# Kernel tuning notes

Hardware: AMD Instinct MI355X
Metric: run time of the kernel (lower is better)

The kernel has to match this reference:

```python
import jax, jax.numpy as jnp
import numpy as np

TAU = 1.0   # ltc_params['tau_constant']
DT = 0.1    # LTCCell default dt
UNFOLDS = 6 # ltc_params['ode_unfolds']
B, S, D, H, O = 512, 512, 128, 128, 1


def setup_inputs() -> dict:
    key = jax.random.key(0)
    ks = jax.random.split(key, 7)
    sc = lambda n: 1.0 / np.sqrt(n)
    return {
        "x":    jax.random.normal(ks[0], (B, S, D), dtype=jnp.float32),
        "W_in": jax.random.normal(ks[1], (H, D), dtype=jnp.float32) * sc(D),
        "b_in": jax.random.normal(ks[2], (H,), dtype=jnp.float32) * sc(D),
        "W_r":  jax.random.normal(ks[3], (H, H), dtype=jnp.float32) * sc(H),
        "b_r":  jax.random.normal(ks[4], (H,), dtype=jnp.float32) * sc(H),
        "W_fc": jax.random.normal(ks[5], (O, H), dtype=jnp.float32) * sc(H),
        "b_fc": jax.random.normal(ks[6], (O,), dtype=jnp.float32) * sc(H),
    }


def reference(x, W_in, b_in, W_r, b_r, W_fc, b_fc):
    # input_map(x[:, t]) is invariant across the inner unfold loop -> precompute once.
    xin_all = jnp.einsum('bsd,hd->bsh', x, W_in) + b_in  # [B,S,H]

    def step(h, xin):  # h: [B,H], xin: [B,H]
        for _ in range(UNFOLDS):  # small fixed count, unrolled
            v = jnp.tanh(xin + h @ W_r.T + b_r)
            h = h + DT * (-h / TAU + v)
        return h, None

    h0 = jnp.zeros((x.shape[0], W_r.shape[0]), dtype=x.dtype)
    h, _ = jax.lax.scan(step, h0, jnp.swapaxes(xin_all, 0, 1))  # scan over seq
    return (h @ W_fc.T + b_fc).squeeze(-1)  # [B]
```

## Files before the change

kernel.cpp:

```cpp
#include <hip/hip_runtime.h>


typedef _Float16 v2h __attribute__((ext_vector_type(2)));

#define S_LEN 512
#define HDIM 128
#define NUNF 6
#define DTC 0.1f

__device__ __forceinline__ float fast_tanh(float y) {
    float u = __expf(2.0f * y);
    return 1.0f - __fdividef(2.0f, u + 1.0f);
}

__global__ __launch_bounds__(256, 2)
void ltc_kernel(const float* __restrict__ x,
                const float* __restrict__ W_in,
                const float* __restrict__ b_in,
                const float* __restrict__ W_r,
                const float* __restrict__ b_r,
                const float* __restrict__ W_fc,
                const float* __restrict__ b_fc,
                float* __restrict__ out)
{
    const int b     = blockIdx.x;
    const int tid   = threadIdx.x;
    const int o     = tid >> 1;
    const int kh    = tid & 1;
    const int kbase = kh * 64;

    __shared__ __align__(16) _Float16 hbuf[2][HDIM];
    __shared__ __align__(16) _Float16 xbuf[2][HDIM];
    __shared__ float red[4];

    v2h wr[32], wi[32];
    {
        const float4* wrp = reinterpret_cast<const float4*>(W_r  + o * HDIM + kbase);
        const float4* wip = reinterpret_cast<const float4*>(W_in + o * HDIM + kbase);
#pragma unroll
        for (int j = 0; j < 16; ++j) {
            float4 f = wrp[j];
            wr[2*j]   = v2h{(_Float16)f.x, (_Float16)f.y};
            wr[2*j+1] = v2h{(_Float16)f.z, (_Float16)f.w};
            float4 g = wip[j];
            wi[2*j]   = v2h{(_Float16)g.x, (_Float16)g.y};
            wi[2*j+1] = v2h{(_Float16)g.z, (_Float16)g.w};
        }
    }
    const float binv = b_in[o];
    const float brv  = b_r[o];

    const float* x_row = x + (size_t)b * S_LEN * HDIM;

    float h_o = 0.0f;

    if (tid < HDIM) {
        xbuf[0][tid] = (_Float16)x_row[tid];
        hbuf[0][tid] = (_Float16)0.0f;
    }
    __syncthreads();

    for (int s = 0; s < S_LEN; ++s) {
        float xnext = 0.0f;
        if (tid < HDIM && s + 1 < S_LEN)
            xnext = x_row[(size_t)(s + 1) * HDIM + tid];

        float xin_o;
        {
            const float4* hp = reinterpret_cast<const float4*>(&xbuf[s & 1][kbase]);
            float4 hv[8];
#pragma unroll
            for (int j = 0; j < 8; ++j) hv[j] = hp[j];
            const v2h* hh = reinterpret_cast<const v2h*>(hv);
            float a0 = 0.f, a1 = 0.f, a2 = 0.f, a3 = 0.f;
#pragma unroll
            for (int j = 0; j < 32; j += 4) {
                a0 = __builtin_amdgcn_fdot2(wi[j],   hh[j],   a0, false);
                a1 = __builtin_amdgcn_fdot2(wi[j+1], hh[j+1], a1, false);
                a2 = __builtin_amdgcn_fdot2(wi[j+2], hh[j+2], a2, false);
                a3 = __builtin_amdgcn_fdot2(wi[j+3], hh[j+3], a3, false);
            }
            float sum = (a0 + a1) + (a2 + a3);
            sum += __shfl_xor(sum, 1);
            xin_o = sum + binv;
        }

#pragma unroll
        for (int u = 0; u < NUNF; ++u) {
            const float4* hp = reinterpret_cast<const float4*>(&hbuf[u & 1][kbase]);
            float4 hv[8];
#pragma unroll
            for (int j = 0; j < 8; ++j) hv[j] = hp[j];
            const v2h* hh = reinterpret_cast<const v2h*>(hv);
            float a0 = 0.f, a1 = 0.f, a2 = 0.f, a3 = 0.f;
#pragma unroll
            for (int j = 0; j < 32; j += 4) {
                a0 = __builtin_amdgcn_fdot2(wr[j],   hh[j],   a0, false);
                a1 = __builtin_amdgcn_fdot2(wr[j+1], hh[j+1], a1, false);
                a2 = __builtin_amdgcn_fdot2(wr[j+2], hh[j+2], a2, false);
                a3 = __builtin_amdgcn_fdot2(wr[j+3], hh[j+3], a3, false);
            }
            float sum = (a0 + a1) + (a2 + a3);
            sum += __shfl_xor(sum, 1);
            float yv = xin_o + brv + sum;
            float v  = fast_tanh(yv);
            h_o = h_o + DTC * (v - h_o);
            if ((tid & 1) == 0)
                hbuf[(u + 1) & 1][o] = (_Float16)h_o;
            if (u == NUNF - 1 && tid < HDIM && s + 1 < S_LEN)
                xbuf[(s + 1) & 1][tid] = (_Float16)xnext;
            __syncthreads();
        }
    }

    float partial = 0.0f;
    if ((tid & 1) == 0) partial = h_o * W_fc[o];
#pragma unroll
    for (int d = 1; d < 64; d <<= 1) partial += __shfl_xor(partial, d);
    if ((tid & 63) == 0) red[tid >> 6] = partial;
    __syncthreads();
    if (tid == 0) out[b] = red[0] + red[1] + red[2] + red[3] + b_fc[0];
}

extern "C" void kernel_launch(void* const* d_in, const int* in_sizes, int n_in,
                              void* d_out, int out_size, void* d_ws, size_t ws_size,
                              hipStream_t stream) {
    const float* x    = (const float*)d_in[0];
    const float* W_in = (const float*)d_in[1];
    const float* b_in = (const float*)d_in[2];
    const float* W_r  = (const float*)d_in[3];
    const float* b_r  = (const float*)d_in[4];
    const float* W_fc = (const float*)d_in[5];
    const float* b_fc = (const float*)d_in[6];
    float* outp = (float*)d_out;
    (void)in_sizes; (void)n_in; (void)out_size; (void)d_ws; (void)ws_size;
    ltc_kernel<<<dim3(512), dim3(256), 0, stream>>>(x, W_in, b_in, W_r, b_r, W_fc, b_fc, outp);
}
```

Before: 1.537 ms.

## Halve block size so each thread computes two output rows

Blocks shrink from 256 to 128 threads. Each thread now holds weight slices for two output rows (o and o+64) and computes two half dot-products per step, then keeps the one matching its k-half. Barriers per block now span two wavefronts instead of four, and every thread writes h with no idle lanes. The cost is double the register weight storage (128 v2h per thread), which raises register pressure and may limit occupancy, plus twice the dot-product work per thread.

```diff
diff --git a/kernel.cpp b/kernel.cpp
--- a/kernel.cpp
+++ b/kernel.cpp
@@ -13,7 +13,7 @@
     return 1.0f - __fdividef(2.0f, u + 1.0f);
 }
 
-__global__ __launch_bounds__(256, 2)
+__global__ __launch_bounds__(128, 2)
 void ltc_kernel(const float* __restrict__ x,
                 const float* __restrict__ W_in,
                 const float* __restrict__ b_in,
@@ -25,64 +25,68 @@
 {
     const int b     = blockIdx.x;
     const int tid   = threadIdx.x;
-    const int o     = tid >> 1;
+    const int og    = tid >> 1;
     const int kh    = tid & 1;
     const int kbase = kh * 64;
+    const int o0    = og;
+    const int o1    = og + 64;
+    const int od    = kh ? o1 : o0;
 
     __shared__ __align__(16) _Float16 hbuf[2][HDIM];
     __shared__ __align__(16) _Float16 xbuf[2][HDIM];
-    __shared__ float red[4];
+    __shared__ float red[2];
 
-    v2h wr[32], wi[32];
+    v2h wr0[32], wr1[32], wi0[32], wi1[32];
     {
-        const float4* wrp = reinterpret_cast<const float4*>(W_r  + o * HDIM + kbase);
-        const float4* wip = reinterpret_cast<const float4*>(W_in + o * HDIM + kbase);
+        const float4* wr0p = reinterpret_cast<const float4*>(W_r  + o0 * HDIM + kbase);
+        const float4* wr1p = reinterpret_cast<const float4*>(W_r  + o1 * HDIM + kbase);
+        const float4* wi0p = reinterpret_cast<const float4*>(W_in + o0 * HDIM + kbase);
+        const float4* wi1p = reinterpret_cast<const float4*>(W_in + o1 * HDIM + kbase);
 #pragma unroll
         for (int j = 0; j < 16; ++j) {
-            float4 f = wrp[j];
-            wr[2*j]   = v2h{(_Float16)f.x, (_Float16)f.y};
-            wr[2*j+1] = v2h{(_Float16)f.z, (_Float16)f.w};
-            float4 g = wip[j];
-            wi[2*j]   = v2h{(_Float16)g.x, (_Float16)g.y};
-            wi[2*j+1] = v2h{(_Float16)g.z, (_Float16)g.w};
+            float4 f;
+            f = wr0p[j]; wr0[2*j] = v2h{(_Float16)f.x,(_Float16)f.y}; wr0[2*j+1] = v2h{(_Float16)f.z,(_Float16)f.w};
+            f = wr1p[j]; wr1[2*j] = v2h{(_Float16)f.x,(_Float16)f.y}; wr1[2*j+1] = v2h{(_Float16)f.z,(_Float16)f.w};
+            f = wi0p[j]; wi0[2*j] = v2h{(_Float16)f.x,(_Float16)f.y}; wi0[2*j+1] = v2h{(_Float16)f.z,(_Float16)f.w};
+            f = wi1p[j]; wi1[2*j] = v2h{(_Float16)f.x,(_Float16)f.y}; wi1[2*j+1] = v2h{(_Float16)f.z,(_Float16)f.w};
         }
     }
-    const float binv = b_in[o];
-    const float brv  = b_r[o];
+    const float binv = b_in[od];
+    const float brv  = b_r[od];
 
     const float* x_row = x + (size_t)b * S_LEN * HDIM;
 
-    float h_o = 0.0f;
+    float h_d = 0.0f;
 
-    if (tid < HDIM) {
-        xbuf[0][tid] = (_Float16)x_row[tid];
-        hbuf[0][tid] = (_Float16)0.0f;
-    }
+    xbuf[0][tid] = (_Float16)x_row[tid];
+    hbuf[0][tid] = (_Float16)0.0f;
     __syncthreads();
 
     for (int s = 0; s < S_LEN; ++s) {
         float xnext = 0.0f;
-        if (tid < HDIM && s + 1 < S_LEN)
+        if (s + 1 < S_LEN)
             xnext = x_row[(size_t)(s + 1) * HDIM + tid];
 
-        float xin_o;
+        float xin_d;
         {
             const float4* hp = reinterpret_cast<const float4*>(&xbuf[s & 1][kbase]);
             float4 hv[8];
 #pragma unroll
             for (int j = 0; j < 8; ++j) hv[j] = hp[j];
             const v2h* hh = reinterpret_cast<const v2h*>(hv);
-            float a0 = 0.f, a1 = 0.f, a2 = 0.f, a3 = 0.f;
+            float a0 = 0.f, a1 = 0.f, b0 = 0.f, b1 = 0.f;
 #pragma unroll
-            for (int j = 0; j < 32; j += 4) {
-                a0 = __builtin_amdgcn_fdot2(wi[j],   hh[j],   a0, false);
-                a1 = __builtin_amdgcn_fdot2(wi[j+1], hh[j+1], a1, false);
-                a2 = __builtin_amdgcn_fdot2(wi[j+2], hh[j+2], a2, false);
-                a3 = __builtin_amdgcn_fdot2(wi[j+3], hh[j+3], a3, false);
+            for (int j = 0; j < 32; j += 2) {
+                a0 = __builtin_amdgcn_fdot2(wi0[j],   hh[j],   a0, false);
+                a1 = __builtin_amdgcn_fdot2(wi0[j+1], hh[j+1], a1, false);
+                b0 = __builtin_amdgcn_fdot2(wi1[j],   hh[j],   b0, false);
+                b1 = __builtin_amdgcn_fdot2(wi1[j+1], hh[j+1], b1, false);
             }
-            float sum = (a0 + a1) + (a2 + a3);
-            sum += __shfl_xor(sum, 1);
-            xin_o = sum + binv;
+            float p0 = a0 + a1;
+            float p1 = b0 + b1;
+            float f0 = p0 + __shfl_xor(p0, 1);
+            float f1 = p1 + __shfl_xor(p1, 1);
+            xin_d = (kh ? f1 : f0) + binv;
         }
 
 #pragma unroll
@@ -92,34 +96,34 @@
 #pragma unroll
             for (int j = 0; j < 8; ++j) hv[j] = hp[j];
             const v2h* hh = reinterpret_cast<const v2h*>(hv);
-            float a0 = 0.f, a1 = 0.f, a2 = 0.f, a3 = 0.f;
+            float a0 = 0.f, a1 = 0.f, b0 = 0.f, b1 = 0.f;
 #pragma unroll
-            for (int j = 0; j < 32; j += 4) {
-                a0 = __builtin_amdgcn_fdot2(wr[j],   hh[j],   a0, false);
-                a1 = __builtin_amdgcn_fdot2(wr[j+1], hh[j+1], a1, false);
-                a2 = __builtin_amdgcn_fdot2(wr[j+2], hh[j+2], a2, false);
-                a3 = __builtin_amdgcn_fdot2(wr[j+3], hh[j+3], a3, false);
+            for (int j = 0; j < 32; j += 2) {
+                a0 = __builtin_amdgcn_fdot2(wr0[j],   hh[j],   a0, false);
+                a1 = __builtin_amdgcn_fdot2(wr0[j+1], hh[j+1], a1, false);
+                b0 = __builtin_amdgcn_fdot2(wr1[j],   hh[j],   b0, false);
+                b1 = __builtin_amdgcn_fdot2(wr1[j+1], hh[j+1], b1, false);
             }
-            float sum = (a0 + a1) + (a2 + a3);
-            sum += __shfl_xor(sum, 1);
-            float yv = xin_o + brv + sum;
+            float p0 = a0 + a1;
+            float p1 = b0 + b1;
+            float f0 = p0 + __shfl_xor(p0, 1);
+            float f1 = p1 + __shfl_xor(p1, 1);
+            float yv = xin_d + brv + (kh ? f1 : f0);
             float v  = fast_tanh(yv);
-            h_o = h_o + DTC * (v - h_o);
-            if ((tid & 1) == 0)
-                hbuf[(u + 1) & 1][o] = (_Float16)h_o;
-            if (u == NUNF - 1 && tid < HDIM && s + 1 < S_LEN)
+            h_d = h_d + DTC * (v - h_d);
+            hbuf[(u + 1) & 1][od] = (_Float16)h_d;
+            if (u == NUNF - 1 && s + 1 < S_LEN)
                 xbuf[(s + 1) & 1][tid] = (_Float16)xnext;
             __syncthreads();
         }
     }
 
-    float partial = 0.0f;
-    if ((tid & 1) == 0) partial = h_o * W_fc[o];
+    float partial = h_d * W_fc[od];
 #pragma unroll
     for (int d = 1; d < 64; d <<= 1) partial += __shfl_xor(partial, d);
     if ((tid & 63) == 0) red[tid >> 6] = partial;
     __syncthreads();
-    if (tid == 0) out[b] = red[0] + red[1] + red[2] + red[3] + b_fc[0];
+    if (tid == 0) out[b] = red[0] + red[1] + b_fc[0];
 }
 
 extern "C" void kernel_launch(void* const* d_in, const int* in_sizes, int n_in,
@@ -134,5 +138,5 @@
     const float* b_fc = (const float*)d_in[6];
     float* outp = (float*)d_out;
     (void)in_sizes; (void)n_in; (void)out_size; (void)d_ws; (void)ws_size;
-    ltc_kernel<<<dim3(512), dim3(256), 0, stream>>>(x, W_in, b_in, W_r, b_r, W_fc, b_fc, outp);
+    ltc_kernel<<<dim3(512), dim3(128), 0, stream>>>(x, W_in, b_in, W_r, b_r, W_fc, b_fc, outp);
 }
```

Result: slower. 1.804 ms (+17.4%).

## Run each batch row on a single wavefront to drop block barriers

Applied to the files above, without the earlier changes.

Each batch row is now handled by one 64-lane wavefront instead of a 256-thread block. Each lane computes two full-length output rows with the fp16 weights held in registers. This removes the per-unfold __syncthreads, the cross-lane shuffle and the double-buffered shared memory, which were serialising the recurrence. In exchange each wave does four times the dot-product work per step, fewer waves are resident per CU, and the roughly 256 VGPRs of weights raise register pressure and the risk of spills.

```diff
diff --git a/kernel.cpp b/kernel.cpp
--- a/kernel.cpp
+++ b/kernel.cpp
@@ -13,7 +13,7 @@
     return 1.0f - __fdividef(2.0f, u + 1.0f);
 }
 
-__global__ __launch_bounds__(256, 2)
+__global__ __launch_bounds__(64, 1)
 void ltc_kernel(const float* __restrict__ x,
                 const float* __restrict__ W_in,
                 const float* __restrict__ b_in,
@@ -23,103 +23,113 @@
                 const float* __restrict__ b_fc,
                 float* __restrict__ out)
 {
-    const int b     = blockIdx.x;
-    const int tid   = threadIdx.x;
-    const int o     = tid >> 1;
-    const int kh    = tid & 1;
-    const int kbase = kh * 64;
+    const int b  = blockIdx.x;
+    const int ln = threadIdx.x;
+    const int o0 = ln;
+    const int o1 = ln + 64;
 
-    __shared__ __align__(16) _Float16 hbuf[2][HDIM];
-    __shared__ __align__(16) _Float16 xbuf[2][HDIM];
-    __shared__ float red[4];
+    __shared__ __align__(16) _Float16 hbuf[HDIM];
+    __shared__ __align__(16) _Float16 xbuf[HDIM];
 
-    v2h wr[32], wi[32];
+    v2h wr0[64], wr1[64], wi0[64], wi1[64];
     {
-        const float4* wrp = reinterpret_cast<const float4*>(W_r  + o * HDIM + kbase);
-        const float4* wip = reinterpret_cast<const float4*>(W_in + o * HDIM + kbase);
+        const float2* r0 = reinterpret_cast<const float2*>(W_r  + o0 * HDIM);
+        const float2* r1 = reinterpret_cast<const float2*>(W_r  + o1 * HDIM);
+        const float2* i0 = reinterpret_cast<const float2*>(W_in + o0 * HDIM);
+        const float2* i1 = reinterpret_cast<const float2*>(W_in + o1 * HDIM);
 #pragma unroll
-        for (int j = 0; j < 16; ++j) {
-            float4 f = wrp[j];
-            wr[2*j]   = v2h{(_Float16)f.x, (_Float16)f.y};
-            wr[2*j+1] = v2h{(_Float16)f.z, (_Float16)f.w};
-            float4 g = wip[j];
-            wi[2*j]   = v2h{(_Float16)g.x, (_Float16)g.y};
-            wi[2*j+1] = v2h{(_Float16)g.z, (_Float16)g.w};
+        for (int p = 0; p < 64; ++p) {
+            float2 f;
+            f = r0[p]; wr0[p] = v2h{(_Float16)f.x, (_Float16)f.y};
+            f = r1[p]; wr1[p] = v2h{(_Float16)f.x, (_Float16)f.y};
+            f = i0[p]; wi0[p] = v2h{(_Float16)f.x, (_Float16)f.y};
+            f = i1[p]; wi1[p] = v2h{(_Float16)f.x, (_Float16)f.y};
         }
     }
-    const float binv = b_in[o];
-    const float brv  = b_r[o];
+    const float bi0 = b_in[o0], bi1 = b_in[o1];
+    const float br0 = b_r[o0],  br1 = b_r[o1];
 
     const float* x_row = x + (size_t)b * S_LEN * HDIM;
 
-    float h_o = 0.0f;
+    float h0 = 0.0f, h1 = 0.0f;
 
-    if (tid < HDIM) {
-        xbuf[0][tid] = (_Float16)x_row[tid];
-        hbuf[0][tid] = (_Float16)0.0f;
-    }
-    __syncthreads();
+    xbuf[o0] = (_Float16)x_row[o0];
+    xbuf[o1] = (_Float16)x_row[o1];
+    hbuf[o0] = (_Float16)0.0f;
+    hbuf[o1] = (_Float16)0.0f;
 
     for (int s = 0; s < S_LEN; ++s) {
-        float xnext = 0.0f;
-        if (tid < HDIM && s + 1 < S_LEN)
-            xnext = x_row[(size_t)(s + 1) * HDIM + tid];
+        float xn0 = 0.0f, xn1 = 0.0f;
+        if (s + 1 < S_LEN) {
+            const float* xr = x_row + (size_t)(s + 1) * HDIM;
+            xn0 = xr[o0];
+            xn1 = xr[o1];
+        }
 
-        float xin_o;
+        float xin0, xin1;
         {
-            const float4* hp = reinterpret_cast<const float4*>(&xbuf[s & 1][kbase]);
-            float4 hv[8];
+            const float4* xp = reinterpret_cast<const float4*>(xbuf);
+            float4 hv[16];
 #pragma unroll
-            for (int j = 0; j < 8; ++j) hv[j] = hp[j];
+            for (int j = 0; j < 16; ++j) hv[j] = xp[j];
             const v2h* hh = reinterpret_cast<const v2h*>(hv);
             float a0 = 0.f, a1 = 0.f, a2 = 0.f, a3 = 0.f;
+            float c0 = 0.f, c1 = 0.f, c2 = 0.f, c3 = 0.f;
 #pragma unroll
-            for (int j = 0; j < 32; j += 4) {
-                a0 = __builtin_amdgcn_fdot2(wi[j],   hh[j],   a0, false);
-                a1 = __builtin_amdgcn_fdot2(wi[j+1], hh[j+1], a1, false);
-                a2 = __builtin_amdgcn_fdot2(wi[j+2], hh[j+2], a2, false);
-                a3 = __builtin_amdgcn_fdot2(wi[j+3], hh[j+3], a3, false);
+            for (int p = 0; p < 64; p += 4) {
+                a0 = __builtin_amdgcn_fdot2(wi0[p],   hh[p],   a0, false);
+                a1 = __builtin_amdgcn_fdot2(wi0[p+1], hh[p+1], a1, false);
+                a2 = __builtin_amdgcn_fdot2(wi0[p+2], hh[p+2], a2, false);
+                a3 = __builtin_amdgcn_fdot2(wi0[p+3], hh[p+3], a3, false);
+                c0 = __builtin_amdgcn_fdot2(wi1[p],   hh[p],   c0, false);
+                c1 = __builtin_amdgcn_fdot2(wi1[p+1], hh[p+1], c1, false);
+                c2 = __builtin_amdgcn_fdot2(wi1[p+2], hh[p+2], c2, false);
+                c3 = __builtin_amdgcn_fdot2(wi1[p+3], hh[p+3], c3, false);
             }
-            float sum = (a0 + a1) + (a2 + a3);
-            sum += __shfl_xor(sum, 1);
-            xin_o = sum + binv;
+            xin0 = (a0 + a1) + (a2 + a3) + bi0;
+            xin1 = (c0 + c1) + (c2 + c3) + bi1;
         }
 
 #pragma unroll
         for (int u = 0; u < NUNF; ++u) {
-            const float4* hp = reinterpret_cast<const float4*>(&hbuf[u & 1][kbase]);
-            float4 hv[8];
+            const float4* hp = reinterpret_cast<const float4*>(hbuf);
+            float4 hv[16];
 #pragma unroll
-            for (int j = 0; j < 8; ++j) hv[j] = hp[j];
+            for (int j = 0; j < 16; ++j) hv[j] = hp[j];
             const v2h* hh = reinterpret_cast<const v2h*>(hv);
             float a0 = 0.f, a1 = 0.f, a2 = 0.f, a3 = 0.f;
+            float c0 = 0.f, c1 = 0.f, c2 = 0.f, c3 = 0.f;
 #pragma unroll
-            for (int j = 0; j < 32; j += 4) {
-                a0 = __builtin_amdgcn_fdot2(wr[j],   hh[j],   a0, false);
-                a1 = __builtin_amdgcn_fdot2(wr[j+1], hh[j+1], a1, false);
-                a2 = __builtin_amdgcn_fdot2(wr[j+2], hh[j+2], a2, false);
-                a3 = __builtin_amdgcn_fdot2(wr[j+3], hh[j+3], a3, false);
+            for (int p = 0; p < 64; p += 4) {
+                a0 = __builtin_amdgcn_fdot2(wr0[p],   hh[p],   a0, false);
+                a1 = __builtin_amdgcn_fdot2(wr0[p+1], hh[p+1], a1, false);
+                a2 = __builtin_amdgcn_fdot2(wr0[p+2], hh[p+2], a2, false);
+                a3 = __builtin_amdgcn_fdot2(wr0[p+3], hh[p+3], a3, false);
+                c0 = __builtin_amdgcn_fdot2(wr1[p],   hh[p],   c0, false);
+                c1 = __builtin_amdgcn_fdot2(wr1[p+1], hh[p+1], c1, false);
+                c2 = __builtin_amdgcn_fdot2(wr1[p+2], hh[p+2], c2, false);
+                c3 = __builtin_amdgcn_fdot2(wr1[p+3], hh[p+3], c3, false);
             }
-            float sum = (a0 + a1) + (a2 + a3);
-            sum += __shfl_xor(sum, 1);
-            float yv = xin_o + brv + sum;
-            float v  = fast_tanh(yv);
-            h_o = h_o + DTC * (v - h_o);
-            if ((tid & 1) == 0)
-                hbuf[(u + 1) & 1][o] = (_Float16)h_o;
-            if (u == NUNF - 1 && tid < HDIM && s + 1 < S_LEN)
-                xbuf[(s + 1) & 1][tid] = (_Float16)xnext;
-            __syncthreads();
+            float s0 = (a0 + a1) + (a2 + a3);
+            float s1 = (c0 + c1) + (c2 + c3);
+            float v0 = fast_tanh(xin0 + br0 + s0);
+            float v1 = fast_tanh(xin1 + br1 + s1);
+            h0 = h0 + DTC * (v0 - h0);
+            h1 = h1 + DTC * (v1 - h1);
+            hbuf[o0] = (_Float16)h0;
+            hbuf[o1] = (_Float16)h1;
+        }
+
+        if (s + 1 < S_LEN) {
+            xbuf[o0] = (_Float16)xn0;
+            xbuf[o1] = (_Float16)xn1;
         }
     }
 
-    float partial = 0.0f;
-    if ((tid & 1) == 0) partial = h_o * W_fc[o];
+    float partial = h0 * W_fc[o0] + h1 * W_fc[o1];
 #pragma unroll
     for (int d = 1; d < 64; d <<= 1) partial += __shfl_xor(partial, d);
-    if ((tid & 63) == 0) red[tid >> 6] = partial;
-    __syncthreads();
-    if (tid == 0) out[b] = red[0] + red[1] + red[2] + red[3] + b_fc[0];
+    if (ln == 0) out[b] = partial + b_fc[0];
 }
 
 extern "C" void kernel_launch(void* const* d_in, const int* in_sizes, int n_in,
@@ -134,5 +144,5 @@
     const float* b_fc = (const float*)d_in[6];
     float* outp = (float*)d_out;
     (void)in_sizes; (void)n_in; (void)out_size; (void)d_ws; (void)ws_size;
-    ltc_kernel<<<dim3(512), dim3(256), 0, stream>>>(x, W_in, b_in, W_r, b_r, W_fc, b_fc, outp);
+    ltc_kernel<<<dim3(512), dim3(64), 0, stream>>>(x, W_in, b_in, W_r, b_r, W_fc, b_fc, outp);
 }
```

Result: slower. 3.204 ms (+108.4%).

## Split input projection into separate kernel and run recurrence in a single wavefront

Applied to the files above, without the earlier changes.

Moves the W_in projection out of the sequential loop into a parallel precompute kernel that writes packed fp16 pairs to workspace. The recurrence kernel then uses one 64-lane wavefront per batch row, each lane owning two hidden units, so there is no __syncthreads and no cross-lane shuffle per unfold. Instead it relies on wavefront-synchronous LDS writes and reads of the hidden state. This trades one barrier per unfold for more serial work per lane and lower occupancy (512 single-wave blocks), and assumes a workspace of 64 MB. Without that workspace it falls back to the old kernel.

```diff
diff --git a/kernel.cpp b/kernel.cpp
--- a/kernel.cpp
+++ b/kernel.cpp
@@ -5,8 +5,13 @@
 
 #define S_LEN 512
 #define HDIM 128
+#define BATCH 512
 #define NUNF 6
 #define DTC 0.1f
+
+__device__ __forceinline__ v2h pk2h(float a, float b) {
+    return __builtin_bit_cast(v2h, __builtin_amdgcn_cvt_pkrtz(a, b));
+}
 
 __device__ __forceinline__ float fast_tanh(float y) {
     float u = __expf(2.0f * y);
@@ -14,15 +19,156 @@
 }
 
 __global__ __launch_bounds__(256, 2)
-void ltc_kernel(const float* __restrict__ x,
+void xin_kernel(const float* __restrict__ x,
                 const float* __restrict__ W_in,
                 const float* __restrict__ b_in,
+                unsigned int* __restrict__ xin)
+{
+    __shared__ __align__(16) _Float16 xt[128 * HDIM];
+    const int tid  = threadIdx.x;
+    const int w    = tid >> 6;
+    const int lane = tid & 63;
+    const int bs0  = blockIdx.x * 128;
+
+    const float4* xg = reinterpret_cast<const float4*>(x + (size_t)bs0 * HDIM);
+#pragma unroll
+    for (int i = 0; i < 16; ++i) {
+        int idx = i * 1024 + tid * 4;
+        float4 v = xg[idx >> 2];
+        v2h* d = reinterpret_cast<v2h*>(xt + idx);
+        d[0] = pk2h(v.x, v.y);
+        d[1] = pk2h(v.z, v.w);
+    }
+
+    v2h wi0[64], wi1[64];
+    {
+        const float4* r0 = reinterpret_cast<const float4*>(W_in + (size_t)lane * HDIM);
+        const float4* r1 = reinterpret_cast<const float4*>(W_in + (size_t)(lane + 64) * HDIM);
+#pragma unroll
+        for (int j = 0; j < 32; ++j) {
+            float4 f = r0[j];
+            wi0[2*j]   = pk2h(f.x, f.y);
+            wi0[2*j+1] = pk2h(f.z, f.w);
+            float4 g = r1[j];
+            wi1[2*j]   = pk2h(g.x, g.y);
+            wi1[2*j+1] = pk2h(g.z, g.w);
+        }
+    }
+    const float bi0 = b_in[lane], bi1 = b_in[lane + 64];
+    __syncthreads();
+
+    for (int rr = 0; rr < 32; ++rr) {
+        const int r = w * 32 + rr;
+        const float4* hp = reinterpret_cast<const float4*>(xt + r * HDIM);
+        float a0 = 0.f, a1 = 0.f, c0 = 0.f, c1 = 0.f;
+#pragma unroll
+        for (int j = 0; j < 16; ++j) {
+            float4 q = hp[j];
+            const v2h* hh = reinterpret_cast<const v2h*>(&q);
+            a0 = __builtin_amdgcn_fdot2(wi0[4*j+0], hh[0], a0, false);
+            a1 = __builtin_amdgcn_fdot2(wi0[4*j+1], hh[1], a1, false);
+            a0 = __builtin_amdgcn_fdot2(wi0[4*j+2], hh[2], a0, false);
+            a1 = __builtin_amdgcn_fdot2(wi0[4*j+3], hh[3], a1, false);
+            c0 = __builtin_amdgcn_fdot2(wi1[4*j+0], hh[0], c0, false);
+            c1 = __builtin_amdgcn_fdot2(wi1[4*j+1], hh[1], c1, false);
+            c0 = __builtin_amdgcn_fdot2(wi1[4*j+2], hh[2], c0, false);
+            c1 = __builtin_amdgcn_fdot2(wi1[4*j+3], hh[3], c1, false);
+        }
+        v2h pk = pk2h(a0 + a1 + bi0, c0 + c1 + bi1);
+        xin[(size_t)(bs0 + r) * 64 + lane] = __builtin_bit_cast(unsigned int, pk);
+    }
+}
+
+__global__ __launch_bounds__(64, 1)
+void ltc_kernel(const unsigned int* __restrict__ xin,
                 const float* __restrict__ W_r,
                 const float* __restrict__ b_r,
                 const float* __restrict__ W_fc,
                 const float* __restrict__ b_fc,
                 float* __restrict__ out)
 {
+    const int b  = blockIdx.x;
+    const int ln = threadIdx.x;
+    const int o0 = ln, o1 = ln + 64;
+
+    __shared__ __align__(16) v2h hbuf[64];
+
+    v2h wr0[64], wr1[64];
+    {
+        const float4* lo0 = reinterpret_cast<const float4*>(W_r + (size_t)o0 * HDIM);
+        const float4* hi0 = reinterpret_cast<const float4*>(W_r + (size_t)o0 * HDIM + 64);
+        const float4* lo1 = reinterpret_cast<const float4*>(W_r + (size_t)o1 * HDIM);
+        const float4* hi1 = reinterpret_cast<const float4*>(W_r + (size_t)o1 * HDIM + 64);
+#pragma unroll
+        for (int j = 0; j < 16; ++j) {
+            float4 a = lo0[j], h = hi0[j];
+            wr0[4*j+0] = pk2h(a.x, h.x);
+            wr0[4*j+1] = pk2h(a.y, h.y);
+            wr0[4*j+2] = pk2h(a.z, h.z);
+            wr0[4*j+3] = pk2h(a.w, h.w);
+            float4 c = lo1[j], d = hi1[j];
+            wr1[4*j+0] = pk2h(c.x, d.x);
+            wr1[4*j+1] = pk2h(c.y, d.y);
+            wr1[4*j+2] = pk2h(c.z, d.z);
+            wr1[4*j+3] = pk2h(c.w, d.w);
+        }
+    }
+    const float br0 = b_r[o0], br1 = b_r[o1];
+    const unsigned int* xrow = xin + (size_t)b * S_LEN * 64;
+
+    float h0 = 0.f, h1 = 0.f;
+    hbuf[ln] = v2h{(_Float16)0.f, (_Float16)0.f};
+    unsigned int xcur = xrow[ln];
+
+    for (int s = 0; s < S_LEN; ++s) {
+        unsigned int xnext = 0;
+        if (s + 1 < S_LEN) xnext = xrow[(s + 1) * 64 + ln];
+        v2h xp = __builtin_bit_cast(v2h, xcur);
+        const float xs0 = (float)xp.x + br0;
+        const float xs1 = (float)xp.y + br1;
+
+#pragma unroll
+        for (int u = 0; u < NUNF; ++u) {
+            const float4* hp = reinterpret_cast<const float4*>(hbuf);
+            float a0 = 0.f, a1 = 0.f, c0 = 0.f, c1 = 0.f;
+#pragma unroll
+            for (int j = 0; j < 16; ++j) {
+                float4 q = hp[j];
+                const v2h* hh = reinterpret_cast<const v2h*>(&q);
+                a0 = __builtin_amdgcn_fdot2(wr0[4*j+0], hh[0], a0, false);
+                a1 = __builtin_amdgcn_fdot2(wr0[4*j+1], hh[1], a1, false);
+                a0 = __builtin_amdgcn_fdot2(wr0[4*j+2], hh[2], a0, false);
+                a1 = __builtin_amdgcn_fdot2(wr0[4*j+3], hh[3], a1, false);
+                c0 = __builtin_amdgcn_fdot2(wr1[4*j+0], hh[0], c0, false);
+                c1 = __builtin_amdgcn_fdot2(wr1[4*j+1], hh[1], c1, false);
+                c0 = __builtin_amdgcn_fdot2(wr1[4*j+2], hh[2], c0, false);
+                c1 = __builtin_amdgcn_fdot2(wr1[4*j+3], hh[3], c1, false);
+            }
+            float v0 = fast_tanh(xs0 + a0 + a1);
+            float v1 = fast_tanh(xs1 + c0 + c1);
+            h0 = h0 + DTC * (v0 - h0);
+            h1 = h1 + DTC * (v1 - h1);
+            hbuf[ln] = pk2h(h0, h1);
+        }
+        xcur = xnext;
+    }
+
+    float partial = h0 * W_fc[o0] + h1 * W_fc[o1];
+#pragma unroll
+    for (int d = 1; d < 64; d <<= 1) partial += __shfl_xor(partial, d);
+    if (ln == 0) out[b] = partial + b_fc[0];
+}
+
+__global__ __launch_bounds__(256, 2)
+void ltc_fallback(const float* __restrict__ x,
+                  const float* __restrict__ W_in,
+                  const float* __restrict__ b_in,
+                  const float* __restrict__ W_r,
+                  const float* __restrict__ b_r,
+                  const float* __restrict__ W_fc,
+                  const float* __restrict__ b_fc,
+                  float* __restrict__ out)
+{
     const int b     = blockIdx.x;
     const int tid   = threadIdx.x;
     const int o     = tid >> 1;
@@ -40,18 +186,16 @@
 #pragma unroll
         for (int j = 0; j < 16; ++j) {
             float4 f = wrp[j];
-            wr[2*j]   = v2h{(_Float16)f.x, (_Float16)f.y};
-            wr[2*j+1] = v2h{(_Float16)f.z, (_Float16)f.w};
+            wr[2*j]   = pk2h(f.x, f.y);
+            wr[2*j+1] = pk2h(f.z, f.w);
             float4 g = wip[j];
-            wi[2*j]   = v2h{(_Float16)g.x, (_Float16)g.y};
-            wi[2*j+1] = v2h{(_Float16)g.z, (_Float16)g.w};
+            wi[2*j]   = pk2h(g.x, g.y);
+            wi[2*j+1] = pk2h(g.z, g.w);
         }
     }
     const float binv = b_in[o];
     const float brv  = b_r[o];
-
     const float* x_row = x + (size_t)b * S_LEN * HDIM;
-
     float h_o = 0.0f;
 
     if (tid < HDIM) {
@@ -133,6 +277,14 @@
     const float* W_fc = (const float*)d_in[5];
     const float* b_fc = (const float*)d_in[6];
     float* outp = (float*)d_out;
-    (void)in_sizes; (void)n_in; (void)out_size; (void)d_ws; (void)ws_size;
-    ltc_kernel<<<dim3(512), dim3(256), 0, stream>>>(x, W_in, b_in, W_r, b_r, W_fc, b_fc, outp);
-}
+    (void)in_sizes; (void)n_in; (void)out_size;
+
+    const size_t need = (size_t)BATCH * S_LEN * 64 * sizeof(unsigned int);
+    if (ws_size >= need) {
+        unsigned int* xin = (unsigned int*)d_ws;
+        xin_kernel<<<dim3(2048), dim3(256), 0, stream>>>(x, W_in, b_in, xin);
+        ltc_kernel<<<dim3(512), dim3(64), 0, stream>>>(xin, W_r, b_r, W_fc, b_fc, outp);
+    } else {
+        ltc_fallback<<<dim3(512), dim3(256), 0, stream>>>(x, W_in, b_in, W_r, b_r, W_fc, b_fc, outp);
+    }
+}
```

Measured after the change: 1.620 ms. 5.4% more time.
